# Optimization experiments

Measured on AMD Instinct MI355X. Metric: run time of the kernel, lower is better.

## Reference

```python
import jax, jax.numpy as jnp
import numpy as np

# Production-scale dims (ScanNet-like 3D instance segmentation, Mask3D-style matcher)
B = 4            # scenes per batch (equal-size segments; offset = cumulative N)
N = 65536        # points per scene
Q = 400          # instance queries
NUM_CLASSES = 20 # semantic classes
M = 64           # max GT instances per scene
COST_CLASS = 1.0
COST_MASK = 1.0
COST_DICE = 1.0


def setup_inputs() -> dict:
    key = jax.random.key(0)
    k1, k2, k3, k4 = jax.random.split(key, 4)
    outputs_mask = jax.random.normal(k1, (B, N, Q), dtype=jnp.float32)
    outputs_class = jax.random.normal(k2, (B, Q, NUM_CLASSES), dtype=jnp.float32)
    instance = jax.random.randint(k3, (B, N), 0, M, dtype=jnp.int32)
    segment = jax.random.randint(k4, (B, N), 0, NUM_CLASSES, dtype=jnp.int32)
    return {
        'outputs_mask': outputs_mask,
        'outputs_class': outputs_class,
        'instance': instance,
        'segment': segment,
    }


def _cost_matrix(out_mask_nq, out_cls, inst, seg):
    # out_mask_nq: [N, Q] mask logits; out_cls: [Q, C]; inst, seg: [N] int
    out_mask = out_mask_nq.T                      # [Q, N]
    out_seg = jax.nn.softmax(out_cls, axis=-1)    # [Q, C]

    # F.one_hot(inst + 1).T[1:] with labels in [0, M) == one_hot(inst, M).T
    tgt = jax.nn.one_hot(inst, M, dtype=jnp.float32).T  # [M, N]

    # semantic label per instance: (tgt_mask * tgt_segm).max(1)
    inst_seg = jnp.max(tgt * seg.astype(jnp.float32)[None, :], axis=1).astype(jnp.int32)  # [M]
    cost_class = 1.0 - out_seg[:, inst_seg]       # [Q, M]

    # batch_sigmoid_ce_loss: BCEwithLogits(x,1)=softplus(-x), BCEwithLogits(x,0)=softplus(x)
    inv_hw = 1.0 / N
    pos = jax.nn.softplus(-out_mask) * inv_hw     # [Q, N]
    neg = jax.nn.softplus(out_mask) * inv_hw      # [Q, N]
    cost_mask = (jnp.einsum('qn,mn->qm', pos, tgt)
                 + jnp.einsum('qn,mn->qm', neg, 1.0 - tgt))  # [Q, M]

    # batch_dice_loss
    sig = jax.nn.sigmoid(out_mask)                # [Q, N]
    numerator = 2.0 * jnp.einsum('qn,mn->qm', sig, tgt)
    denominator = sig.sum(-1)[:, None] + tgt.sum(-1)[None, :]
    cost_dice = 1.0 - (numerator + 1.0) / (denominator + 1.0)

    return COST_MASK * cost_mask + COST_CLASS * cost_class + COST_DICE * cost_dice


def reference(outputs_mask, outputs_class, instance, segment):
    # vmap over scenes (equal-size segments replace the per-batch offset loop)
    return jax.vmap(_cost_matrix)(outputs_mask, outputs_class, instance, segment)  # [B, Q, M]
```

## Files before the change

### kernel.cpp

```cpp
#include <hip/hip_runtime.h>
#include <hip/hip_bf16.h>

#define B_ 4
#define N_ 65536
#define Q_ 400
#define C_ 20
#define M_ 64
#define QT 64
#define CHUNK 2048
#define NCHUNK (N_ / CHUNK)
#define NQT ((Q_ + QT - 1) / QT)
#define OFFSTRIDE (M_ + 2)

#define SX 8192.0f
#define SS 32768.0f
#define SN 8192.0f

__global__ __launch_bounds__(256) void sort_kernel(const int* __restrict__ inst,
                                                   const int* __restrict__ seg,
                                                   unsigned short* __restrict__ perm,
                                                   int* __restrict__ binoff,
                                                   int* __restrict__ cnt_g,
                                                   int* __restrict__ smax_g) {
    int b = blockIdx.x >> 5;
    int chunk = blockIdx.x & 31;
    __shared__ int hist[M_];
    __shared__ int smax[M_];
    __shared__ int cur[M_];
    __shared__ int off[M_ + 1];
    __shared__ unsigned short lperm[CHUNK];
    int tid = threadIdx.x;
    if (tid < M_) { hist[tid] = 0; smax[tid] = 0; }
    __syncthreads();

    int base = b * N_ + chunk * CHUNK;
    int mloc[CHUNK / 256];
#pragma unroll
    for (int i = 0; i < CHUNK / 256; ++i) {
        int idx = tid + i * 256;
        int m = inst[base + idx];
        int s = seg[base + idx];
        mloc[i] = m;
        atomicAdd(&hist[m], 1);
        atomicMax(&smax[m], s);
    }
    __syncthreads();

    if (tid == 0) {
        int acc = 0;
        for (int m = 0; m < M_; ++m) { off[m] = acc; acc += hist[m]; }
        off[M_] = acc;
    }
    __syncthreads();
    if (tid < M_) cur[tid] = off[tid];
    __syncthreads();

#pragma unroll
    for (int i = 0; i < CHUNK / 256; ++i) {
        int idx = tid + i * 256;
        int pos = atomicAdd(&cur[mloc[i]], 1);
        lperm[pos] = (unsigned short)idx;
    }
    __syncthreads();

    unsigned int* pg = (unsigned int*)(perm + ((size_t)b * NCHUNK + chunk) * CHUNK);
    const unsigned int* pl = (const unsigned int*)lperm;
    for (int i = tid; i < CHUNK / 2; i += 256) pg[i] = pl[i];

    int obase = (b * NCHUNK + chunk) * OFFSTRIDE;
    if (tid <= M_) binoff[obase + tid] = off[tid];
    if (tid < M_) {
        atomicAdd(&cnt_g[b * M_ + tid], hist[tid]);
        atomicMax(&smax_g[b * M_ + tid], smax[tid]);
    }
}

__global__ __launch_bounds__(512) void bin_kernel(const float* __restrict__ mask,
                                                  const unsigned short* __restrict__ perm,
                                                  const int* __restrict__ binoff,
                                                  int* __restrict__ xsum,
                                                  int* __restrict__ ssum,
                                                  int* __restrict__ negsum) {
    int chunk = blockIdx.x, qt = blockIdx.y, b = blockIdx.z;
    __shared__ unsigned short lperm[CHUNK];
    __shared__ int loff[M_ + 1];
    int tid = threadIdx.x;

    const unsigned int* pg = (const unsigned int*)(perm + ((size_t)b * NCHUNK + chunk) * CHUNK);
    unsigned int* pl = (unsigned int*)lperm;
    for (int i = tid; i < CHUNK / 2; i += 512) pl[i] = pg[i];
    if (tid <= M_) loff[tid] = binoff[(b * NCHUNK + chunk) * OFFSTRIDE + tid];
    __syncthreads();

    int lane = tid & 63, wave = tid >> 6;
    int r = lane >> 4, c = lane & 15;
    int q0 = qt * QT + 4 * c;
    bool qok = (q0 < Q_);
    const float* mbase = mask + ((size_t)b * N_ + (size_t)chunk * CHUNK) * Q_ + q0;
    float n0 = 0.f, n1 = 0.f, n2 = 0.f, n3 = 0.f;

    if (qok) {
        for (int k = 0; k < M_ / 8; ++k) {
            int m = wave + 8 * k;
            int s = loff[m], e = loff[m + 1];
            float x0 = 0.f, x1 = 0.f, x2 = 0.f, x3 = 0.f;
            float g0 = 0.f, g1 = 0.f, g2 = 0.f, g3 = 0.f;
            int pos = s + r;
            for (; pos + 4 < e; pos += 8) {
                int na = lperm[pos];
                int nb = lperm[pos + 4];
                float4 xa = *(const float4*)(mbase + (size_t)na * Q_);
                float4 xb = *(const float4*)(mbase + (size_t)nb * Q_);

                float ea0 = __expf(xa.x), ea1 = __expf(xa.y), ea2 = __expf(xa.z), ea3 = __expf(xa.w);
                float eb0 = __expf(xb.x), eb1 = __expf(xb.y), eb2 = __expf(xb.z), eb3 = __expf(xb.w);
                float ta0 = 1.f + ea0, ta1 = 1.f + ea1, ta2 = 1.f + ea2, ta3 = 1.f + ea3;
                float tb0 = 1.f + eb0, tb1 = 1.f + eb1, tb2 = 1.f + eb2, tb3 = 1.f + eb3;

                x0 += xa.x + xb.x; x1 += xa.y + xb.y;
                x2 += xa.z + xb.z; x3 += xa.w + xb.w;
                g0 += ea0 * __builtin_amdgcn_rcpf(ta0) + eb0 * __builtin_amdgcn_rcpf(tb0);
                g1 += ea1 * __builtin_amdgcn_rcpf(ta1) + eb1 * __builtin_amdgcn_rcpf(tb1);
                g2 += ea2 * __builtin_amdgcn_rcpf(ta2) + eb2 * __builtin_amdgcn_rcpf(tb2);
                g3 += ea3 * __builtin_amdgcn_rcpf(ta3) + eb3 * __builtin_amdgcn_rcpf(tb3);
                n0 += __logf(ta0) + __logf(tb0);
                n1 += __logf(ta1) + __logf(tb1);
                n2 += __logf(ta2) + __logf(tb2);
                n3 += __logf(ta3) + __logf(tb3);
            }
            if (pos < e) {
                int na = lperm[pos];
                float4 xa = *(const float4*)(mbase + (size_t)na * Q_);
                float ea0 = __expf(xa.x), ea1 = __expf(xa.y), ea2 = __expf(xa.z), ea3 = __expf(xa.w);
                float ta0 = 1.f + ea0, ta1 = 1.f + ea1, ta2 = 1.f + ea2, ta3 = 1.f + ea3;
                x0 += xa.x; x1 += xa.y; x2 += xa.z; x3 += xa.w;
                g0 += ea0 * __builtin_amdgcn_rcpf(ta0);
                g1 += ea1 * __builtin_amdgcn_rcpf(ta1);
                g2 += ea2 * __builtin_amdgcn_rcpf(ta2);
                g3 += ea3 * __builtin_amdgcn_rcpf(ta3);
                n0 += __logf(ta0); n1 += __logf(ta1);
                n2 += __logf(ta2); n3 += __logf(ta3);
            }
            x0 += __shfl_xor(x0, 16); x0 += __shfl_xor(x0, 32);
            x1 += __shfl_xor(x1, 16); x1 += __shfl_xor(x1, 32);
            x2 += __shfl_xor(x2, 16); x2 += __shfl_xor(x2, 32);
            x3 += __shfl_xor(x3, 16); x3 += __shfl_xor(x3, 32);
            g0 += __shfl_xor(g0, 16); g0 += __shfl_xor(g0, 32);
            g1 += __shfl_xor(g1, 16); g1 += __shfl_xor(g1, 32);
            g2 += __shfl_xor(g2, 16); g2 += __shfl_xor(g2, 32);
            g3 += __shfl_xor(g3, 16); g3 += __shfl_xor(g3, 32);
            if (r == 0) {
                int bq = ((b * Q_ + q0) << 6) + m;
                atomicAdd(&xsum[bq + (0 << 6)], __float2int_rn(x0 * SX));
                atomicAdd(&xsum[bq + (1 << 6)], __float2int_rn(x1 * SX));
                atomicAdd(&xsum[bq + (2 << 6)], __float2int_rn(x2 * SX));
                atomicAdd(&xsum[bq + (3 << 6)], __float2int_rn(x3 * SX));
                atomicAdd(&ssum[bq + (0 << 6)], (int)__float2uint_rn(g0 * SS));
                atomicAdd(&ssum[bq + (1 << 6)], (int)__float2uint_rn(g1 * SS));
                atomicAdd(&ssum[bq + (2 << 6)], (int)__float2uint_rn(g2 * SS));
                atomicAdd(&ssum[bq + (3 << 6)], (int)__float2uint_rn(g3 * SS));
            }
        }
        n0 += __shfl_xor(n0, 16); n0 += __shfl_xor(n0, 32);
        n1 += __shfl_xor(n1, 16); n1 += __shfl_xor(n1, 32);
        n2 += __shfl_xor(n2, 16); n2 += __shfl_xor(n2, 32);
        n3 += __shfl_xor(n3, 16); n3 += __shfl_xor(n3, 32);
        if (r == 0) {
            atomicAdd(&negsum[b * Q_ + q0 + 0], __float2int_rn(n0 * SN));
            atomicAdd(&negsum[b * Q_ + q0 + 1], __float2int_rn(n1 * SN));
            atomicAdd(&negsum[b * Q_ + q0 + 2], __float2int_rn(n2 * SN));
            atomicAdd(&negsum[b * Q_ + q0 + 3], __float2int_rn(n3 * SN));
        }
    }
}

__global__ __launch_bounds__(64) void final_kernel(const float* __restrict__ cls_in,
                                                   const int* __restrict__ xsum,
                                                   const int* __restrict__ ssum,
                                                   const int* __restrict__ negsum,
                                                   const int* __restrict__ cnt_g,
                                                   const int* __restrict__ smax_g,
                                                   float* __restrict__ out) {
    int bq = blockIdx.x;
    int b = bq / Q_;
    int m = threadIdx.x;
    float Xs = (float)xsum[(bq << 6) + m] * (1.0f / SX);
    float Ss = (float)ssum[(bq << 6) + m] * (1.0f / SS);
    float sigsum = Ss;
    for (int off = 32; off; off >>= 1) sigsum += __shfl_xor(sigsum, off);

    __shared__ float cls[C_];
    if (m < C_) cls[m] = cls_in[bq * C_ + m];
    __syncthreads();
    float mx = cls[0];
    for (int i = 1; i < C_; ++i) mx = fmaxf(mx, cls[i]);
    float se = 0.f;
    for (int i = 0; i < C_; ++i) se += __expf(cls[i] - mx);
    int label = smax_g[b * M_ + m];
    float p = __expf(cls[label] - mx) / se;

    float negf = (float)negsum[bq] * (1.0f / SN);
    float cm = (negf - Xs) * (1.f / (float)N_);
    float cd = 1.f - (2.f * Ss + 1.f) / (sigsum + (float)cnt_g[b * M_ + m] + 1.f);
    out[(bq << 6) + m] = cm + (1.f - p) + cd;
}

extern "C" void kernel_launch(void* const* d_in, const int* in_sizes, int n_in,
                              void* d_out, int out_size, void* d_ws, size_t ws_size,
                              hipStream_t stream) {
    const float* mask = (const float*)d_in[0];
    const float* cls  = (const float*)d_in[1];
    const int*   inst = (const int*)d_in[2];
    const int*   seg  = (const int*)d_in[3];
    float* out = (float*)d_out;

    int* xsum   = (int*)d_ws;
    int* ssum   = xsum + B_ * Q_ * M_;
    int* negsum = ssum + B_ * Q_ * M_;
    int* cnt_g  = negsum + B_ * Q_;
    int* smax_g = cnt_g + B_ * M_;
    int* binoff = smax_g + B_ * M_;
    unsigned short* perm = (unsigned short*)(binoff + B_ * NCHUNK * OFFSTRIDE);

    size_t zbytes = (size_t)(2 * B_ * Q_ * M_ + B_ * Q_ + 2 * B_ * M_) * 4;
    hipMemsetAsync(d_ws, 0, zbytes, stream);

    sort_kernel<<<B_ * NCHUNK, 256, 0, stream>>>(inst, seg, perm, binoff, cnt_g, smax_g);
    bin_kernel<<<dim3(NCHUNK, NQT, B_), 512, 0, stream>>>(mask, perm, binoff, xsum, ssum, negsum);
    final_kernel<<<B_ * Q_, 64, 0, stream>>>(cls, xsum, ssum, negsum, cnt_g, smax_g, out);
}
```

Baseline: 752.1 us.

## Assign one instance bin per lane group, split bins across grid, pack atomics

The bin kernel's work mapping changes. Each wave no longer loops over 8 bins with a cross-lane reduction after each one. Instead each 16-lane row owns one instance bin and walks all of its points serially with a 4-way unrolled load loop, and the grid z dimension is doubled so each block handles half of the bins. The x-sum and sigmoid-sum fixed-point accumulators are packed into one 64-bit word so a single atomic replaces two, and the per-bin shuffle reductions are removed. The trade-off is load imbalance across lanes when bin sizes differ, plus reliance on the low 32-bit field never carrying into the high field.

```diff
diff --git a/kernel.cpp b/kernel.cpp
--- a/kernel.cpp
+++ b/kernel.cpp
@@ -15,6 +15,9 @@
 #define SX 8192.0f
 #define SS 32768.0f
 #define SN 8192.0f
+
+#define PACK(x, g) ((((unsigned long long)(unsigned int)__float2int_rn((x) * SX)) << 32) \
+                    | (unsigned long long)(unsigned int)__float2uint_rn((g) * SS))
 
 __global__ __launch_bounds__(256) void sort_kernel(const int* __restrict__ inst,
                                                    const int* __restrict__ seg,
@@ -78,10 +81,10 @@
 __global__ __launch_bounds__(512) void bin_kernel(const float* __restrict__ mask,
                                                   const unsigned short* __restrict__ perm,
                                                   const int* __restrict__ binoff,
-                                                  int* __restrict__ xsum,
-                                                  int* __restrict__ ssum,
+                                                  unsigned long long* __restrict__ xs_packed,
                                                   int* __restrict__ negsum) {
-    int chunk = blockIdx.x, qt = blockIdx.y, b = blockIdx.z;
+    int chunk = blockIdx.x, qt = blockIdx.y;
+    int b = blockIdx.z >> 1, mhalf = blockIdx.z & 1;
     __shared__ unsigned short lperm[CHUNK];
     __shared__ int loff[M_ + 1];
     int tid = threadIdx.x;
@@ -94,73 +97,47 @@
 
     int lane = tid & 63, wave = tid >> 6;
     int r = lane >> 4, c = lane & 15;
+    int m = mhalf * 32 + wave * 4 + r;
     int q0 = qt * QT + 4 * c;
     bool qok = (q0 < Q_);
     const float* mbase = mask + ((size_t)b * N_ + (size_t)chunk * CHUNK) * Q_ + q0;
+
+    float x0 = 0.f, x1 = 0.f, x2 = 0.f, x3 = 0.f;
+    float g0 = 0.f, g1 = 0.f, g2 = 0.f, g3 = 0.f;
     float n0 = 0.f, n1 = 0.f, n2 = 0.f, n3 = 0.f;
 
+#define ACC4(v) { \
+    float e0 = __expf(v.x), e1 = __expf(v.y), e2 = __expf(v.z), e3 = __expf(v.w); \
+    float t0 = 1.f + e0, t1 = 1.f + e1, t2 = 1.f + e2, t3 = 1.f + e3; \
+    x0 += v.x; x1 += v.y; x2 += v.z; x3 += v.w; \
+    g0 += e0 * __builtin_amdgcn_rcpf(t0); g1 += e1 * __builtin_amdgcn_rcpf(t1); \
+    g2 += e2 * __builtin_amdgcn_rcpf(t2); g3 += e3 * __builtin_amdgcn_rcpf(t3); \
+    n0 += __logf(t0); n1 += __logf(t1); n2 += __logf(t2); n3 += __logf(t3); }
+
     if (qok) {
-        for (int k = 0; k < M_ / 8; ++k) {
-            int m = wave + 8 * k;
-            int s = loff[m], e = loff[m + 1];
-            float x0 = 0.f, x1 = 0.f, x2 = 0.f, x3 = 0.f;
-            float g0 = 0.f, g1 = 0.f, g2 = 0.f, g3 = 0.f;
-            int pos = s + r;
-            for (; pos + 4 < e; pos += 8) {
-                int na = lperm[pos];
-                int nb = lperm[pos + 4];
-                float4 xa = *(const float4*)(mbase + (size_t)na * Q_);
-                float4 xb = *(const float4*)(mbase + (size_t)nb * Q_);
-
-                float ea0 = __expf(xa.x), ea1 = __expf(xa.y), ea2 = __expf(xa.z), ea3 = __expf(xa.w);
-                float eb0 = __expf(xb.x), eb1 = __expf(xb.y), eb2 = __expf(xb.z), eb3 = __expf(xb.w);
-                float ta0 = 1.f + ea0, ta1 = 1.f + ea1, ta2 = 1.f + ea2, ta3 = 1.f + ea3;
-                float tb0 = 1.f + eb0, tb1 = 1.f + eb1, tb2 = 1.f + eb2, tb3 = 1.f + eb3;
-
-                x0 += xa.x + xb.x; x1 += xa.y + xb.y;
-                x2 += xa.z + xb.z; x3 += xa.w + xb.w;
-                g0 += ea0 * __builtin_amdgcn_rcpf(ta0) + eb0 * __builtin_amdgcn_rcpf(tb0);
-                g1 += ea1 * __builtin_amdgcn_rcpf(ta1) + eb1 * __builtin_amdgcn_rcpf(tb1);
-                g2 += ea2 * __builtin_amdgcn_rcpf(ta2) + eb2 * __builtin_amdgcn_rcpf(tb2);
-                g3 += ea3 * __builtin_amdgcn_rcpf(ta3) + eb3 * __builtin_amdgcn_rcpf(tb3);
-                n0 += __logf(ta0) + __logf(tb0);
-                n1 += __logf(ta1) + __logf(tb1);
-                n2 += __logf(ta2) + __logf(tb2);
-                n3 += __logf(ta3) + __logf(tb3);
-            }
-            if (pos < e) {
-                int na = lperm[pos];
-                float4 xa = *(const float4*)(mbase + (size_t)na * Q_);
-                float ea0 = __expf(xa.x), ea1 = __expf(xa.y), ea2 = __expf(xa.z), ea3 = __expf(xa.w);
-                float ta0 = 1.f + ea0, ta1 = 1.f + ea1, ta2 = 1.f + ea2, ta3 = 1.f + ea3;
-                x0 += xa.x; x1 += xa.y; x2 += xa.z; x3 += xa.w;
-                g0 += ea0 * __builtin_amdgcn_rcpf(ta0);
-                g1 += ea1 * __builtin_amdgcn_rcpf(ta1);
-                g2 += ea2 * __builtin_amdgcn_rcpf(ta2);
-                g3 += ea3 * __builtin_amdgcn_rcpf(ta3);
-                n0 += __logf(ta0); n1 += __logf(ta1);
-                n2 += __logf(ta2); n3 += __logf(ta3);
-            }
-            x0 += __shfl_xor(x0, 16); x0 += __shfl_xor(x0, 32);
-            x1 += __shfl_xor(x1, 16); x1 += __shfl_xor(x1, 32);
-            x2 += __shfl_xor(x2, 16); x2 += __shfl_xor(x2, 32);
-            x3 += __shfl_xor(x3, 16); x3 += __shfl_xor(x3, 32);
-            g0 += __shfl_xor(g0, 16); g0 += __shfl_xor(g0, 32);
-            g1 += __shfl_xor(g1, 16); g1 += __shfl_xor(g1, 32);
-            g2 += __shfl_xor(g2, 16); g2 += __shfl_xor(g2, 32);
-            g3 += __shfl_xor(g3, 16); g3 += __shfl_xor(g3, 32);
-            if (r == 0) {
-                int bq = ((b * Q_ + q0) << 6) + m;
-                atomicAdd(&xsum[bq + (0 << 6)], __float2int_rn(x0 * SX));
-                atomicAdd(&xsum[bq + (1 << 6)], __float2int_rn(x1 * SX));
-                atomicAdd(&xsum[bq + (2 << 6)], __float2int_rn(x2 * SX));
-                atomicAdd(&xsum[bq + (3 << 6)], __float2int_rn(x3 * SX));
-                atomicAdd(&ssum[bq + (0 << 6)], (int)__float2uint_rn(g0 * SS));
-                atomicAdd(&ssum[bq + (1 << 6)], (int)__float2uint_rn(g1 * SS));
-                atomicAdd(&ssum[bq + (2 << 6)], (int)__float2uint_rn(g2 * SS));
-                atomicAdd(&ssum[bq + (3 << 6)], (int)__float2uint_rn(g3 * SS));
-            }
+        int s = loff[m], e = loff[m + 1];
+        int pos = s;
+        for (; pos + 3 < e; pos += 4) {
+            int ia = lperm[pos], ib = lperm[pos + 1];
+            int ic = lperm[pos + 2], id = lperm[pos + 3];
+            float4 va = *(const float4*)(mbase + (size_t)ia * Q_);
+            float4 vb = *(const float4*)(mbase + (size_t)ib * Q_);
+            float4 vc = *(const float4*)(mbase + (size_t)ic * Q_);
+            float4 vd = *(const float4*)(mbase + (size_t)id * Q_);
+            ACC4(va) ACC4(vb) ACC4(vc) ACC4(vd)
         }
+        for (; pos < e; ++pos) {
+            int ia = lperm[pos];
+            float4 va = *(const float4*)(mbase + (size_t)ia * Q_);
+            ACC4(va)
+        }
+
+        unsigned long long* dst = xs_packed + (size_t)(((b * Q_ + q0) << 6) + m);
+        atomicAdd(dst + (0 << 6), PACK(x0, g0));
+        atomicAdd(dst + (1 << 6), PACK(x1, g1));
+        atomicAdd(dst + (2 << 6), PACK(x2, g2));
+        atomicAdd(dst + (3 << 6), PACK(x3, g3));
+
         n0 += __shfl_xor(n0, 16); n0 += __shfl_xor(n0, 32);
         n1 += __shfl_xor(n1, 16); n1 += __shfl_xor(n1, 32);
         n2 += __shfl_xor(n2, 16); n2 += __shfl_xor(n2, 32);
@@ -172,11 +149,11 @@
             atomicAdd(&negsum[b * Q_ + q0 + 3], __float2int_rn(n3 * SN));
         }
     }
+#undef ACC4
 }
 
 __global__ __launch_bounds__(64) void final_kernel(const float* __restrict__ cls_in,
-                                                   const int* __restrict__ xsum,
-                                                   const int* __restrict__ ssum,
+                                                   const unsigned long long* __restrict__ xs_packed,
                                                    const int* __restrict__ negsum,
                                                    const int* __restrict__ cnt_g,
                                                    const int* __restrict__ smax_g,
@@ -184,8 +161,9 @@
     int bq = blockIdx.x;
     int b = bq / Q_;
     int m = threadIdx.x;
-    float Xs = (float)xsum[(bq << 6) + m] * (1.0f / SX);
-    float Ss = (float)ssum[(bq << 6) + m] * (1.0f / SS);
+    unsigned long long v = xs_packed[(bq << 6) + m];
+    float Xs = (float)(int)(v >> 32) * (1.0f / SX);
+    float Ss = (float)(unsigned int)(v & 0xffffffffull) * (1.0f / SS);
     float sigsum = Ss;
     for (int off = 32; off; off >>= 1) sigsum += __shfl_xor(sigsum, off);
 
@@ -214,18 +192,17 @@
     const int*   seg  = (const int*)d_in[3];
     float* out = (float*)d_out;
 
-    int* xsum   = (int*)d_ws;
-    int* ssum   = xsum + B_ * Q_ * M_;
-    int* negsum = ssum + B_ * Q_ * M_;
+    unsigned long long* xs_packed = (unsigned long long*)d_ws;
+    int* negsum = (int*)(xs_packed + B_ * Q_ * M_);
     int* cnt_g  = negsum + B_ * Q_;
     int* smax_g = cnt_g + B_ * M_;
     int* binoff = smax_g + B_ * M_;
     unsigned short* perm = (unsigned short*)(binoff + B_ * NCHUNK * OFFSTRIDE);
 
-    size_t zbytes = (size_t)(2 * B_ * Q_ * M_ + B_ * Q_ + 2 * B_ * M_) * 4;
+    size_t zbytes = (size_t)B_ * Q_ * M_ * 8 + (size_t)(B_ * Q_ + 2 * B_ * M_) * 4;
     hipMemsetAsync(d_ws, 0, zbytes, stream);
 
     sort_kernel<<<B_ * NCHUNK, 256, 0, stream>>>(inst, seg, perm, binoff, cnt_g, smax_g);
-    bin_kernel<<<dim3(NCHUNK, NQT, B_), 512, 0, stream>>>(mask, perm, binoff, xsum, ssum, negsum);
-    final_kernel<<<B_ * Q_, 64, 0, stream>>>(cls, xsum, ssum, negsum, cnt_g, smax_g, out);
-}
+    bin_kernel<<<dim3(NCHUNK, NQT, B_ * 2), 512, 0, stream>>>(mask, perm, binoff, xs_packed, negsum);
+    final_kernel<<<B_ * Q_, 64, 0, stream>>>(cls, xs_packed, negsum, cnt_g, smax_g, out);
+}
```

Result: faster. 615.7 us (-18.1%).
